# Performance work log

Hardware: AMD Instinct MI355X
Metric: run time of the kernel (lower is better)

The kernel has to match this reference:

```python
import jax, jax.numpy as jnp
import numpy as np

D_IN, D, P, H, DH, DFF, L = 3072, 1024, 36, 8, 128, 2048, 6
SCALE = np.float32(1.0 / np.sqrt(DH))
# leave-one-out index matrix: row i lists all patch indices except i -> (36, 35)
LOO_IDX = jnp.asarray(np.array([[j for j in range(P) if j != i] for i in range(P)], dtype=np.int32))


def _ln(x, g, b, eps=1e-5):
    m = jnp.mean(x, axis=-1, keepdims=True)
    v = jnp.var(x, axis=-1, keepdims=True)
    return (x - m) / jnp.sqrt(v + eps) * g + b


def setup_inputs() -> dict:
    key = jax.random.key(0)
    ks = jax.random.split(key, 16)
    w = lambda k, shape: jax.random.normal(k, shape, jnp.float32) * 0.02
    return {
        "x": jax.random.normal(ks[0], (128, P, D_IN), jnp.float32),
        "ln0_g": jnp.ones((D_IN,), jnp.float32), "ln0_b": jnp.zeros((D_IN,), jnp.float32),
        "Wred": w(ks[1], (D, D_IN)), "bred": jnp.zeros((D,), jnp.float32),
        "h0_w1": w(ks[2], (64, D)), "h0_b1": jnp.zeros((64,), jnp.float32),
        "h0_w2": w(ks[3], (1, 64)), "h0_b2": jnp.zeros((1,), jnp.float32),
        "temperature": jnp.ones((1,), jnp.float32) * 0.07,
        "Wqkv": w(ks[4], (L, 3 * D, D)), "bqkv": jnp.zeros((L, 3 * D), jnp.float32),
        "Wo": w(ks[5], (L, D, D)), "bo": jnp.zeros((L, D), jnp.float32),
        "ln1_g": jnp.ones((L, D), jnp.float32), "ln1_b": jnp.zeros((L, D), jnp.float32),
        "W1": w(ks[6], (L, DFF, D)), "b1": jnp.zeros((L, DFF), jnp.float32),
        "W2": w(ks[7], (L, D, DFF)), "b2": jnp.zeros((L, D), jnp.float32),
        "ln2_g": jnp.ones((L, D), jnp.float32), "ln2_b": jnp.zeros((L, D), jnp.float32),
        "lnf_g": jnp.ones((D,), jnp.float32), "lnf_b": jnp.zeros((D,), jnp.float32),
    }


def reference(x, ln0_g, ln0_b, Wred, bred, h0_w1, h0_b1, h0_w2, h0_b2, temperature,
              Wqkv, bqkv, Wo, bo, ln1_g, ln1_b, W1, b1, W2, b2, ln2_g, ln2_b, lnf_g, lnf_b):
    B = x.shape[0]
    # dim_reduce (dropout is identity at inference)
    xr = jax.nn.gelu(_ln(x, ln0_g, ln0_b) @ Wred.T + bred, approximate=False)  # (B,P,D)

    # Leave-one-out attention maps. H0 is a pointwise (kernel_size=1) stack,
    # so each position's score is independent: compute once, then gather the
    h1 = jax.nn.gelu(jnp.einsum('bpc,oc->bpo', xr, h0_w1) + h0_b1, approximate=False)  # (B,P,64)
    full = jnp.einsum('bpo,uo->bpu', h1, h0_w2)[..., 0] + h0_b2[0]                      # (B,P)
    attention_maps = jax.nn.sigmoid(full[:, LOO_IDX] / temperature[0])                  # (B,P,P-1)

    # Pre-norm transformer encoder (PyTorch norm_first=True, relu FFN, no final encoder norm)
    y = xr
    for l in range(L):
        qkv = _ln(y, ln1_g[l], ln1_b[l]) @ Wqkv[l].T + bqkv[l]  # (B,P,3D)
        q, k, v = jnp.split(qkv, 3, axis=-1)
        q = q.reshape(B, P, H, DH).transpose(0, 2, 1, 3)
        k = k.reshape(B, P, H, DH).transpose(0, 2, 1, 3)
        v = v.reshape(B, P, H, DH).transpose(0, 2, 1, 3)
        attn = jax.nn.softmax(jnp.einsum('bhqd,bhkd->bhqk', q, k) * SCALE, axis=-1)
        o = jnp.einsum('bhqk,bhkd->bhqd', attn, v).transpose(0, 2, 1, 3).reshape(B, P, D)
        y = y + o @ Wo[l].T + bo[l]
        f = jax.nn.relu(_ln(y, ln2_g[l], ln2_b[l]) @ W1[l].T + b1[l])
        y = y + f @ W2[l].T + b2[l]

    return _ln(y, lnf_g, lnf_b), attention_maps
```

## Files before the change

kernel.cpp:

```cpp
#include <hip/hip_runtime.h>
#include <hip/hip_bf16.h>

typedef unsigned short u16;
typedef unsigned int u32;
typedef __bf16 bf16x8 __attribute__((ext_vector_type(8)));
typedef float f32x4 __attribute__((ext_vector_type(4)));

#define DEV static __device__ __forceinline__
#define GPTR(p) (const __attribute__((address_space(1))) u32*)(p)
#define LPTR(p) (__attribute__((address_space(3))) u32*)(p)

DEV float bf2f(u16 u) { return __uint_as_float((u32)u << 16); }
DEV u16 f2bf(float f) {
  u32 x = __float_as_uint(f);
  x += 0x7fffu + ((x >> 16) & 1u);
  return (u16)(x >> 16);
}
DEV float gelu_f(float x) { return 0.5f * x * (1.0f + erff(x * 0.70710678118654752440f)); }

__global__ void cvt_k(const float* __restrict__ in, u16* __restrict__ out, int n4) {
  int i = blockIdx.x * 256 + threadIdx.x;
  if (i < n4) {
    float4 v = ((const float4*)in)[i];
    ushort4 o;
    o.x = f2bf(v.x); o.y = f2bf(v.y); o.z = f2bf(v.z); o.w = f2bf(v.w);
    ((ushort4*)out)[i] = o;
  }
}

__global__ void w1t_k(const float* __restrict__ w1, float* __restrict__ w1t) {
  int i = blockIdx.x * 256 + threadIdx.x;
  if (i < 64 * 1024) {
    int o = i >> 10, c = i & 1023;
    w1t[c * 64 + o] = w1[i];
  }
}

template<int DIM, int OUTM, int INBF>
__global__ __launch_bounds__(256) void ln_k(const void* __restrict__ inp,
                                            const float* __restrict__ g,
                                            const float* __restrict__ b,
                                            void* __restrict__ outp) {
  constexpr int NV = DIM / 1024;
  const int row = blockIdx.x, tid = threadIdx.x;
  float4 v[NV];
  float s = 0.f, s2 = 0.f;
#pragma unroll
  for (int i = 0; i < NV; ++i) {
    if (INBF == 0) {
      v[i] = ((const float4*)inp)[(size_t)row * (DIM / 4) + tid + i * 256];
    } else {
      ushort4 u = ((const ushort4*)inp)[(size_t)row * (DIM / 4) + tid + i * 256];
      v[i] = make_float4(bf2f(u.x), bf2f(u.y), bf2f(u.z), bf2f(u.w));
    }
    s += v[i].x + v[i].y + v[i].z + v[i].w;
    s2 += v[i].x * v[i].x + v[i].y * v[i].y + v[i].z * v[i].z + v[i].w * v[i].w;
  }
  __shared__ float red[8];
#pragma unroll
  for (int off = 32; off; off >>= 1) { s += __shfl_down(s, off); s2 += __shfl_down(s2, off); }
  if ((tid & 63) == 0) { red[(tid >> 6) * 2] = s; red[(tid >> 6) * 2 + 1] = s2; }
  __syncthreads();
  s = red[0] + red[2] + red[4] + red[6];
  s2 = red[1] + red[3] + red[5] + red[7];
  const float mean = s / DIM;
  const float rstd = rsqrtf(s2 / DIM - mean * mean + 1e-5f);
#pragma unroll
  for (int i = 0; i < NV; ++i) {
    const int c4 = tid + i * 256;
    float4 gv = ((const float4*)g)[c4];
    float4 bv = ((const float4*)b)[c4];
    float o0 = (v[i].x - mean) * rstd * gv.x + bv.x;
    float o1 = (v[i].y - mean) * rstd * gv.y + bv.y;
    float o2 = (v[i].z - mean) * rstd * gv.z + bv.z;
    float o3 = (v[i].w - mean) * rstd * gv.w + bv.w;
    if (OUTM == 0) {
      ushort4 u4;
      u4.x = f2bf(o0); u4.y = f2bf(o1); u4.z = f2bf(o2); u4.w = f2bf(o3);
      ((ushort4*)outp)[(size_t)row * (DIM / 4) + c4] = u4;
    } else {
      ((float4*)outp)[(size_t)row * (DIM / 4) + c4] = make_float4(o0, o1, o2, o3);
    }
  }
}

template<int EPI, int BN>
__global__ __launch_bounds__(512, BN == 64 ? 6 : 4)
void gemm_bt(const u16* __restrict__ A,
             const u16* __restrict__ B,
             const float* __restrict__ bias,
             u16* __restrict__ Cb,
             int N, int K, int nx) {
  constexpr int WC = BN / 32;
  constexpr int MR = (128 * WC / 8) / 16;
  __shared__ u16 As[2][128 * 64];
  __shared__ u16 Bs[2][BN * 64];
  const int tid = threadIdx.x;
  const int nwg = gridDim.x;
  const int bid = blockIdx.x;
  const int swz = (bid & 7) * (nwg >> 3) + (bid >> 3);
  const int by = swz / nx, bx = swz - by * nx;
  const int brow = by * 128, bcol = bx * BN;
  const int lane = tid & 63, w = tid >> 6;
  const int wr = (w / WC) * (MR * 16), wc = (w % WC) * 32;
  const int fr = lane & 15, fg = lane >> 4;
  const int swb = (fr & 7) << 4;
  const int ldr = lane >> 3;
  const int lc8 = lane & 7;
  const int cs8 = (lc8 ^ ldr) * 8;

  const u16* Ab = A + (size_t)(brow + ldr) * K + cs8;
  const u16* Bb = B + (size_t)(bcol + ldr) * K + cs8;

  f32x4 acc[MR][2];
  const f32x4 z = {0.f, 0.f, 0.f, 0.f};
#pragma unroll
  for (int m = 0; m < MR; ++m) { acc[m][0] = z; acc[m][1] = z; }

  auto stage = [&](int kt, int buf) {
    const int k0 = kt << 6;
#pragma unroll
    for (int i = 0; i < 2; ++i) {
      const int c = i * 8 + w;
      __builtin_amdgcn_global_load_lds(GPTR(Ab + (size_t)c * 8 * K + k0),
                                       LPTR(&As[buf][c * 512 + lane * 8]), 16, 0, 0);
    }
#pragma unroll
    for (int i = 0; i < BN / 64; ++i) {
      const int c = i * 8 + w;
      __builtin_amdgcn_global_load_lds(GPTR(Bb + (size_t)c * 8 * K + k0),
                                       LPTR(&Bs[buf][c * 512 + lane * 8]), 16, 0, 0);
    }
  };

  stage(0, 0);
  const int nkt = K >> 6;
  for (int kt = 0; kt < nkt; ++kt) {
    const int buf = kt & 1;
    asm volatile("s_waitcnt vmcnt(0)" ::: "memory");
    __builtin_amdgcn_s_barrier();
    __builtin_amdgcn_sched_barrier(0);
    if (kt + 1 < nkt) stage(kt + 1, buf ^ 1);
    const char* Asb = (const char*)&As[buf][0];
    const char* Bsb = (const char*)&Bs[buf][0];
    __builtin_amdgcn_s_setprio(1);
#pragma unroll
    for (int ks = 0; ks < 2; ++ks) {
      bf16x8 af[MR], bfr[2];
      const int cb = (ks * 64 + fg * 16) ^ swb;
#pragma unroll
      for (int m = 0; m < MR; ++m)
        af[m] = *(const bf16x8*)(Asb + (wr + m * 16 + fr) * 128 + cb);
#pragma unroll
      for (int n = 0; n < 2; ++n)
        bfr[n] = *(const bf16x8*)(Bsb + (wc + n * 16 + fr) * 128 + cb);
#pragma unroll
      for (int m = 0; m < MR; ++m)
#pragma unroll
        for (int n = 0; n < 2; ++n)
          acc[m][n] = __builtin_amdgcn_mfma_f32_16x16x32_bf16(af[m], bfr[n], acc[m][n], 0, 0, 0);
    }
    __builtin_amdgcn_s_setprio(0);
  }

#pragma unroll
  for (int n = 0; n < 2; ++n) {
    const int col = bcol + wc + n * 16 + fr;
    const float bv = bias[col];
#pragma unroll
    for (int m = 0; m < MR; ++m) {
      const int row0 = brow + wr + m * 16 + fg * 4;
#pragma unroll
      for (int j = 0; j < 4; ++j) {
        float v = acc[m][n][j] + bv;
        const size_t idx = (size_t)(row0 + j) * N + col;
        if (EPI == 0) Cb[idx] = f2bf(gelu_f(v));
        else if (EPI == 1) Cb[idx] = f2bf(v);
        else if (EPI == 2) Cb[idx] = f2bf(bf2f(Cb[idx]) + v);
        else Cb[idx] = f2bf(fmaxf(v, 0.f));
      }
    }
  }
}

__global__ __launch_bounds__(256) void attn_k(const u16* __restrict__ qkv, u16* __restrict__ o) {
  constexpr int LDQ = 136;
  __shared__ u16 Q[36 * LDQ], Kk[36 * LDQ], V[36 * LDQ];
  __shared__ float S[36][38];
  const int tid = threadIdx.x;
  const int b = blockIdx.x >> 3, h = blockIdx.x & 7;
  const size_t base = (size_t)b * 36 * 3072 + h * 128;
  for (int i = tid; i < 36 * 16; i += 256) {
    const int r = i >> 4, c = (i & 15) << 3;
    const size_t src = base + (size_t)r * 3072 + c;
    *(uint4*)&Q[r * LDQ + c] = *(const uint4*)&qkv[src];
    *(uint4*)&Kk[r * LDQ + c] = *(const uint4*)&qkv[src + 1024];
    *(uint4*)&V[r * LDQ + c] = *(const uint4*)&qkv[src + 2048];
  }
  __syncthreads();
  for (int i = tid; i < 36 * 36; i += 256) {
    const int r = i / 36, c = i - r * 36;
    float s = 0.f;
    for (int d = 0; d < 128; ++d) s += bf2f(Q[r * LDQ + d]) * bf2f(Kk[c * LDQ + d]);
    S[r][c] = s * 0.08838834764831845f;
  }
  __syncthreads();
  if (tid < 36) {
    float mx = -1e30f;
    for (int c = 0; c < 36; ++c) mx = fmaxf(mx, S[tid][c]);
    float sum = 0.f;
    for (int c = 0; c < 36; ++c) { float e = expf(S[tid][c] - mx); S[tid][c] = e; sum += e; }
    const float inv = 1.f / sum;
    for (int c = 0; c < 36; ++c) S[tid][c] *= inv;
  }
  __syncthreads();
  for (int i = tid; i < 36 * 16; i += 256) {
    const int r = i >> 4, d0 = (i & 15) << 3;
    float s[8] = {0.f, 0.f, 0.f, 0.f, 0.f, 0.f, 0.f, 0.f};
    for (int j = 0; j < 36; ++j) {
      const float p = S[r][j];
#pragma unroll
      for (int e = 0; e < 8; ++e) s[e] += p * bf2f(V[j * LDQ + d0 + e]);
    }
    uint4 pk;
    pk.x = (u32)f2bf(s[0]) | ((u32)f2bf(s[1]) << 16);
    pk.y = (u32)f2bf(s[2]) | ((u32)f2bf(s[3]) << 16);
    pk.z = (u32)f2bf(s[4]) | ((u32)f2bf(s[5]) << 16);
    pk.w = (u32)f2bf(s[6]) | ((u32)f2bf(s[7]) << 16);
    *(uint4*)&o[(size_t)(b * 36 + r) * 1024 + h * 128 + d0] = pk;
  }
}

__global__ __launch_bounds__(256) void h0_k(const u16* __restrict__ xr,
                                            const float* __restrict__ w1t,
                                            const float* __restrict__ b1,
                                            const float* __restrict__ w2,
                                            const float* __restrict__ b2v,
                                            float* __restrict__ full) {
  __shared__ float xs[8][1024];
  const int t0 = blockIdx.x * 8, tid = threadIdx.x;
#pragma unroll
  for (int i = 0; i < 8; ++i) {
    const int idx = tid + i * 256;
    const int t = idx >> 8, c4 = idx & 255;
    ushort4 u = ((const ushort4*)(xr + (size_t)(t0 + t) * 1024))[c4];
    xs[t][c4 * 4 + 0] = bf2f(u.x);
    xs[t][c4 * 4 + 1] = bf2f(u.y);
    xs[t][c4 * 4 + 2] = bf2f(u.z);
    xs[t][c4 * 4 + 3] = bf2f(u.w);
  }
  __syncthreads();
  const int w = tid >> 6, lane = tid & 63;
  float s0 = 0.f, s1 = 0.f;
  for (int c = 0; c < 1024; ++c) {
    const float wv = w1t[c * 64 + lane];
    s0 = fmaf(xs[w * 2 + 0][c], wv, s0);
    s1 = fmaf(xs[w * 2 + 1][c], wv, s1);
  }
  const float bb = b1[lane], wo = w2[lane];
  float v0 = gelu_f(s0 + bb) * wo;
  float v1 = gelu_f(s1 + bb) * wo;
#pragma unroll
  for (int off = 32; off; off >>= 1) {
    v0 += __shfl_down(v0, off);
    v1 += __shfl_down(v1, off);
  }
  if (lane == 0) {
    full[t0 + w * 2 + 0] = v0 + b2v[0];
    full[t0 + w * 2 + 1] = v1 + b2v[0];
  }
}

__global__ void am2_k(const float* __restrict__ full, const float* __restrict__ temp,
                      float* __restrict__ out) {
  const int i = blockIdx.x * 256 + threadIdx.x;
  if (i < 128 * 36 * 35) {
    const int j = i % 35;
    const int t = i / 35;
    const int p = t % 36;
    const int b = t / 36;
    const int col = j + (j >= p ? 1 : 0);
    const float v = full[b * 36 + col] / temp[0];
    out[i] = 1.f / (1.f + expf(-v));
  }
}

extern "C" void kernel_launch(void* const* d_in, const int* in_sizes, int n_in,
                              void* d_out, int out_size, void* d_ws, size_t ws_size,
                              hipStream_t stream) {
  const float* x     = (const float*)d_in[0];
  const float* ln0_g = (const float*)d_in[1];
  const float* ln0_b = (const float*)d_in[2];
  const float* Wred  = (const float*)d_in[3];
  const float* bred  = (const float*)d_in[4];
  const float* h0_w1 = (const float*)d_in[5];
  const float* h0_b1 = (const float*)d_in[6];
  const float* h0_w2 = (const float*)d_in[7];
  const float* h0_b2 = (const float*)d_in[8];
  const float* temp  = (const float*)d_in[9];
  const float* Wqkv  = (const float*)d_in[10];
  const float* bqkv  = (const float*)d_in[11];
  const float* Wo    = (const float*)d_in[12];
  const float* bo    = (const float*)d_in[13];
  const float* ln1_g = (const float*)d_in[14];
  const float* ln1_b = (const float*)d_in[15];
  const float* W1    = (const float*)d_in[16];
  const float* b1    = (const float*)d_in[17];
  const float* W2    = (const float*)d_in[18];
  const float* b2    = (const float*)d_in[19];
  const float* ln2_g = (const float*)d_in[20];
  const float* ln2_b = (const float*)d_in[21];
  const float* lnf_g = (const float*)d_in[22];
  const float* lnf_b = (const float*)d_in[23];

  char* ws = (char*)d_ws;
  size_t off = 0;
  auto alloc = [&](size_t bytes) -> void* {
    void* p = ws + off;
    off += (bytes + 255) & ~(size_t)255;
    return p;
  };
  u16* WredB  = (u16*)alloc((size_t)1024 * 3072 * 2);
  u16* WqkvB  = (u16*)alloc((size_t)6 * 3072 * 1024 * 2);
  u16* WoB    = (u16*)alloc((size_t)6 * 1024 * 1024 * 2);
  u16* W1B    = (u16*)alloc((size_t)6 * 2048 * 1024 * 2);
  u16* W2B    = (u16*)alloc((size_t)6 * 1024 * 2048 * 2);
  float* w1t  = (float*)alloc((size_t)1024 * 64 * 4);
  u16* yb     = (u16*)alloc((size_t)4608 * 1024 * 2);
  u16* big    = (u16*)alloc((size_t)4608 * 3072 * 2);
  u16* nbuf   = (u16*)alloc((size_t)4608 * 1024 * 2);
  float* fullb = (float*)alloc((size_t)4608 * 4);

  auto cvt = [&](const float* src, u16* dst, size_t n) {
    int n4 = (int)(n / 4);
    cvt_k<<<(n4 + 255) / 256, 256, 0, stream>>>(src, dst, n4);
  };
  cvt(Wred, WredB, (size_t)1024 * 3072);
  cvt(Wqkv, WqkvB, (size_t)6 * 3072 * 1024);
  cvt(Wo,   WoB,   (size_t)6 * 1024 * 1024);
  cvt(W1,   W1B,   (size_t)6 * 2048 * 1024);
  cvt(W2,   W2B,   (size_t)6 * 1024 * 2048);
  w1t_k<<<64 * 1024 / 256, 256, 0, stream>>>(h0_w1, w1t);

  ln_k<3072, 0, 0><<<4608, 256, 0, stream>>>(x, ln0_g, ln0_b, big);
  gemm_bt<0, 64><<<16 * 36, 512, 0, stream>>>(big, WredB, bred, yb, 1024, 3072, 16);
  h0_k<<<576, 256, 0, stream>>>(yb, w1t, h0_b1, h0_w2, h0_b2, fullb);
  am2_k<<<(128 * 36 * 35 + 255) / 256, 256, 0, stream>>>(fullb, temp,
                                                         (float*)d_out + 4608 * 1024);

  for (int l = 0; l < 6; ++l) {
    ln_k<1024, 0, 1><<<4608, 256, 0, stream>>>(yb, ln1_g + l * 1024, ln1_b + l * 1024, nbuf);
    gemm_bt<1, 128><<<24 * 36, 512, 0, stream>>>(nbuf, WqkvB + (size_t)l * 3072 * 1024,
                                                 bqkv + l * 3072, big, 3072, 1024, 24);
    attn_k<<<128 * 8, 256, 0, stream>>>(big, nbuf);
    gemm_bt<2, 64><<<16 * 36, 512, 0, stream>>>(nbuf, WoB + (size_t)l * 1024 * 1024,
                                                bo + l * 1024, yb, 1024, 1024, 16);
    ln_k<1024, 0, 1><<<4608, 256, 0, stream>>>(yb, ln2_g + l * 1024, ln2_b + l * 1024, nbuf);
    gemm_bt<3, 128><<<16 * 36, 512, 0, stream>>>(nbuf, W1B + (size_t)l * 2048 * 1024,
                                                 b1 + l * 2048, big, 2048, 1024, 16);
    gemm_bt<2, 64><<<16 * 36, 512, 0, stream>>>(big, W2B + (size_t)l * 1024 * 2048,
                                                b2 + l * 1024, yb, 1024, 2048, 16);
  }
  ln_k<1024, 1, 1><<<4608, 256, 0, stream>>>(yb, lnf_g, lnf_b, d_out);
}
```

Baseline: 1.218 ms.

## Rewrite attention with MFMA bf16 matmuls and merge weight conversions into one kernel

The attention kernel now gives each wavefront one head and computes QK^T and PV with 16x16x32 bf16 MFMA instructions instead of scalar LDS dot products. Softmax runs in registers using cross-lane shuffles, and P plus transposed V are staged in padded, zero-filled LDS. Separately, the five fp32-to-bf16 weight conversion launches are merged into one grid-stride kernel to cut launch count. The new attention path rounds the probabilities to bf16 before PV and reads Q/K straight from global memory, which may change numerics slightly.

```diff
diff --git a/kernel.cpp b/kernel.cpp
--- a/kernel.cpp
+++ b/kernel.cpp
@@ -18,13 +18,33 @@
 }
 DEV float gelu_f(float x) { return 0.5f * x * (1.0f + erff(x * 0.70710678118654752440f)); }
 
-__global__ void cvt_k(const float* __restrict__ in, u16* __restrict__ out, int n4) {
-  int i = blockIdx.x * 256 + threadIdx.x;
-  if (i < n4) {
-    float4 v = ((const float4*)in)[i];
+__global__ void cvt5_k(const float* __restrict__ s0, const float* __restrict__ s1,
+                       const float* __restrict__ s2, const float* __restrict__ s3,
+                       const float* __restrict__ s4,
+                       u16* __restrict__ d0, u16* __restrict__ d1, u16* __restrict__ d2,
+                       u16* __restrict__ d3, u16* __restrict__ d4,
+                       int n0, int n1, int n2, int n3, int n4) {
+  const int total = n0 + n1 + n2 + n3 + n4;
+  for (int i = blockIdx.x * 256 + threadIdx.x; i < total; i += gridDim.x * 256) {
+    const float* s; u16* d; int j = i;
+    if (j < n0) { s = s0; d = d0; }
+    else {
+      j -= n0;
+      if (j < n1) { s = s1; d = d1; }
+      else {
+        j -= n1;
+        if (j < n2) { s = s2; d = d2; }
+        else {
+          j -= n2;
+          if (j < n3) { s = s3; d = d3; }
+          else { j -= n3; s = s4; d = d4; }
+        }
+      }
+    }
+    float4 v = ((const float4*)s)[j];
     ushort4 o;
     o.x = f2bf(v.x); o.y = f2bf(v.y); o.z = f2bf(v.z); o.w = f2bf(v.w);
-    ((ushort4*)out)[i] = o;
+    ((ushort4*)d)[j] = o;
   }
 }
 
@@ -183,51 +203,114 @@
   }
 }
 
-__global__ __launch_bounds__(256) void attn_k(const u16* __restrict__ qkv, u16* __restrict__ o) {
-  constexpr int LDQ = 136;
-  __shared__ u16 Q[36 * LDQ], Kk[36 * LDQ], V[36 * LDQ];
-  __shared__ float S[36][38];
-  const int tid = threadIdx.x;
-  const int b = blockIdx.x >> 3, h = blockIdx.x & 7;
-  const size_t base = (size_t)b * 36 * 3072 + h * 128;
-  for (int i = tid; i < 36 * 16; i += 256) {
-    const int r = i >> 4, c = (i & 15) << 3;
-    const size_t src = base + (size_t)r * 3072 + c;
-    *(uint4*)&Q[r * LDQ + c] = *(const uint4*)&qkv[src];
-    *(uint4*)&Kk[r * LDQ + c] = *(const uint4*)&qkv[src + 1024];
-    *(uint4*)&V[r * LDQ + c] = *(const uint4*)&qkv[src + 2048];
-  }
-  __syncthreads();
-  for (int i = tid; i < 36 * 36; i += 256) {
-    const int r = i / 36, c = i - r * 36;
-    float s = 0.f;
-    for (int d = 0; d < 128; ++d) s += bf2f(Q[r * LDQ + d]) * bf2f(Kk[c * LDQ + d]);
-    S[r][c] = s * 0.08838834764831845f;
-  }
-  __syncthreads();
-  if (tid < 36) {
-    float mx = -1e30f;
-    for (int c = 0; c < 36; ++c) mx = fmaxf(mx, S[tid][c]);
-    float sum = 0.f;
-    for (int c = 0; c < 36; ++c) { float e = expf(S[tid][c] - mx); S[tid][c] = e; sum += e; }
-    const float inv = 1.f / sum;
-    for (int c = 0; c < 36; ++c) S[tid][c] *= inv;
-  }
-  __syncthreads();
-  for (int i = tid; i < 36 * 16; i += 256) {
-    const int r = i >> 4, d0 = (i & 15) << 3;
-    float s[8] = {0.f, 0.f, 0.f, 0.f, 0.f, 0.f, 0.f, 0.f};
-    for (int j = 0; j < 36; ++j) {
-      const float p = S[r][j];
-#pragma unroll
-      for (int e = 0; e < 8; ++e) s[e] += p * bf2f(V[j * LDQ + d0 + e]);
-    }
-    uint4 pk;
-    pk.x = (u32)f2bf(s[0]) | ((u32)f2bf(s[1]) << 16);
-    pk.y = (u32)f2bf(s[2]) | ((u32)f2bf(s[3]) << 16);
-    pk.z = (u32)f2bf(s[4]) | ((u32)f2bf(s[5]) << 16);
-    pk.w = (u32)f2bf(s[6]) | ((u32)f2bf(s[7]) << 16);
-    *(uint4*)&o[(size_t)(b * 36 + r) * 1024 + h * 128 + d0] = pk;
+__global__ __launch_bounds__(128) void attn_k(const u16* __restrict__ qkv,
+                                              u16* __restrict__ o) {
+  __shared__ u16 lds[2][12672];
+  const int tid = threadIdx.x, w = tid >> 6, l = tid & 63;
+  const int b = blockIdx.x >> 2, hp = blockIdx.x & 3;
+  const int h = hp * 2 + w;
+  u16* Vt = &lds[w][0];
+  u16* P  = &lds[w][9216];
+  const int fr = l & 15, fg = l >> 4;
+  const size_t qbase = (size_t)b * 36 * 3072 + h * 128;
+  const size_t kbase = qbase + 1024;
+  const size_t vbase = qbase + 2048;
+
+  for (int i = l; i < 1584; i += 64) {
+    uint4 zz = {0u, 0u, 0u, 0u};
+    *(uint4*)&lds[w][i * 8] = zz;
+  }
+
+  for (int i = l; i < 576; i += 64) {
+    const int k = i >> 4, nc = (i & 15) * 8;
+    uint4 u = *(const uint4*)&qkv[vbase + (size_t)k * 3072 + nc];
+    const u16* e = (const u16*)&u;
+#pragma unroll
+    for (int t = 0; t < 8; ++t) Vt[(nc + t) * 72 + k] = e[t];
+  }
+
+  const f32x4 z = {0.f, 0.f, 0.f, 0.f};
+  f32x4 S[3][3];
+#pragma unroll
+  for (int mt = 0; mt < 3; ++mt)
+#pragma unroll
+    for (int nt = 0; nt < 3; ++nt) S[mt][nt] = z;
+#pragma unroll
+  for (int ks = 0; ks < 4; ++ks) {
+    bf16x8 qa[3], kb[3];
+#pragma unroll
+    for (int mt = 0; mt < 3; ++mt) {
+      const int r = min(mt * 16 + fr, 35);
+      qa[mt] = *(const bf16x8*)&qkv[qbase + (size_t)r * 3072 + ks * 32 + fg * 8];
+      kb[mt] = *(const bf16x8*)&qkv[kbase + (size_t)r * 3072 + ks * 32 + fg * 8];
+    }
+#pragma unroll
+    for (int mt = 0; mt < 3; ++mt)
+#pragma unroll
+      for (int nt = 0; nt < 3; ++nt)
+        S[mt][nt] = __builtin_amdgcn_mfma_f32_16x16x32_bf16(qa[mt], kb[nt], S[mt][nt], 0, 0, 0);
+  }
+
+  const float sc = 0.08838834764831845f;
+#pragma unroll
+  for (int mt = 0; mt < 3; ++mt) {
+#pragma unroll
+    for (int j = 0; j < 4; ++j) {
+      float v0 = S[mt][0][j] * sc;
+      float v1 = S[mt][1][j] * sc;
+      float v2 = (fr >= 4) ? -1e30f : S[mt][2][j] * sc;
+      float m = fmaxf(fmaxf(v0, v1), v2);
+#pragma unroll
+      for (int d = 1; d < 16; d <<= 1) m = fmaxf(m, __shfl_xor(m, d));
+      float e0 = __expf(v0 - m);
+      float e1 = __expf(v1 - m);
+      float e2 = (fr >= 4) ? 0.f : __expf(v2 - m);
+      float sum = e0 + e1 + e2;
+#pragma unroll
+      for (int d = 1; d < 16; d <<= 1) sum += __shfl_xor(sum, d);
+      const float inv = 1.f / sum;
+      const int r = mt * 16 + fg * 4 + j;
+      P[r * 72 + fr]      = f2bf(e0 * inv);
+      P[r * 72 + 16 + fr] = f2bf(e1 * inv);
+      P[r * 72 + 32 + fr] = f2bf(e2 * inv);
+    }
+  }
+
+#pragma unroll
+  for (int g = 0; g < 2; ++g) {
+    f32x4 O[3][4];
+#pragma unroll
+    for (int mt = 0; mt < 3; ++mt)
+#pragma unroll
+      for (int nt = 0; nt < 4; ++nt) O[mt][nt] = z;
+#pragma unroll
+    for (int ks = 0; ks < 2; ++ks) {
+      bf16x8 pa[3], vb[4];
+#pragma unroll
+      for (int mt = 0; mt < 3; ++mt)
+        pa[mt] = *(const bf16x8*)&P[(mt * 16 + fr) * 72 + ks * 32 + fg * 8];
+#pragma unroll
+      for (int nt = 0; nt < 4; ++nt)
+        vb[nt] = *(const bf16x8*)&Vt[((g * 4 + nt) * 16 + fr) * 72 + ks * 32 + fg * 8];
+#pragma unroll
+      for (int mt = 0; mt < 3; ++mt)
+#pragma unroll
+        for (int nt = 0; nt < 4; ++nt)
+          O[mt][nt] = __builtin_amdgcn_mfma_f32_16x16x32_bf16(pa[mt], vb[nt], O[mt][nt], 0, 0, 0);
+    }
+#pragma unroll
+    for (int mt = 0; mt < 3; ++mt) {
+#pragma unroll
+      for (int j = 0; j < 4; ++j) {
+        const int r = mt * 16 + fg * 4 + j;
+        if (r < 36) {
+#pragma unroll
+          for (int nt = 0; nt < 4; ++nt)
+            o[((size_t)b * 36 + r) * 1024 + h * 128 + g * 64 + nt * 16 + fr] =
+                f2bf(O[mt][nt][j]);
+        }
+      }
+    }
   }
 }
 
@@ -331,15 +414,10 @@
   u16* nbuf   = (u16*)alloc((size_t)4608 * 1024 * 2);
   float* fullb = (float*)alloc((size_t)4608 * 4);
 
-  auto cvt = [&](const float* src, u16* dst, size_t n) {
-    int n4 = (int)(n / 4);
-    cvt_k<<<(n4 + 255) / 256, 256, 0, stream>>>(src, dst, n4);
-  };
-  cvt(Wred, WredB, (size_t)1024 * 3072);
-  cvt(Wqkv, WqkvB, (size_t)6 * 3072 * 1024);
-  cvt(Wo,   WoB,   (size_t)6 * 1024 * 1024);
-  cvt(W1,   W1B,   (size_t)6 * 2048 * 1024);
-  cvt(W2,   W2B,   (size_t)6 * 1024 * 2048);
+  cvt5_k<<<2048, 256, 0, stream>>>(
+      Wred, Wqkv, Wo, W1, W2, WredB, WqkvB, WoB, W1B, W2B,
+      (int)(1024 * 3072 / 4), (int)(6 * 3072 * 1024 / 4), (int)(6 * 1024 * 1024 / 4),
+      (int)(6 * 2048 * 1024 / 4), (int)(6 * 1024 * 2048 / 4));
   w1t_k<<<64 * 1024 / 256, 256, 0, stream>>>(h0_w1, w1t);
 
   ln_k<3072, 0, 0><<<4608, 256, 0, stream>>>(x, ln0_g, ln0_b, big);
@@ -352,7 +430,7 @@
     ln_k<1024, 0, 1><<<4608, 256, 0, stream>>>(yb, ln1_g + l * 1024, ln1_b + l * 1024, nbuf);
     gemm_bt<1, 128><<<24 * 36, 512, 0, stream>>>(nbuf, WqkvB + (size_t)l * 3072 * 1024,
                                                  bqkv + l * 3072, big, 3072, 1024, 24);
-    attn_k<<<128 * 8, 256, 0, stream>>>(big, nbuf);
+    attn_k<<<128 * 4, 128, 0, stream>>>(big, nbuf);
     gemm_bt<2, 64><<<16 * 36, 512, 0, stream>>>(nbuf, WoB + (size_t)l * 1024 * 1024,
                                                 bo + l * 1024, yb, 1024, 1024, 16);
     ln_k<1024, 0, 1><<<4608, 256, 0, stream>>>(yb, ln2_g + l * 1024, ln2_b + l * 1024, nbuf);
```

Result: faster. 1.134 ms (-6.9%).
